# Performance work log

Hardware: AMD Instinct MI355X
Metric: run time of the kernel (lower is better)

The kernel has to match this reference:

```python
import jax, jax.numpy as jnp
import numpy as np

EPS = 1.1920928955078125e-07  # torch fp32 default eps for F.rms_norm
N_HEADS = 16
HEAD_DIM = 128


def apply_rotary_emb(x, cos, sin):
    # x: [B,S,H,D]; cos/sin: [1,S,1,D/2]
    d = x.shape[-1] // 2
    x1, x2 = x[..., :d], x[..., d:]
    return jnp.concatenate([x1 * cos + x2 * sin, -x1 * sin + x2 * cos], axis=-1)


def rms_norm(x):
    # F.rms_norm over last dim, no learned weight
    ms = jnp.mean(jnp.square(x), axis=-1, keepdims=True)
    return x * jax.lax.rsqrt(ms + EPS)


def setup_inputs() -> dict:
    key = jax.random.key(0)
    ks = jax.random.split(key, 7)
    B, S, D = 2, 2048, 2048
    half = HEAD_DIM // 2
    # rotary tables (built like standard RoPE for realism)
    inv_freq = 1.0 / (10000.0 ** (np.arange(0, half, dtype=np.float32) / half))
    t = np.arange(S, dtype=np.float32)
    freqs = np.outer(t, inv_freq)  # [S, D/2]
    cos = jnp.asarray(np.cos(freqs))[None, :, None, :]
    sin = jnp.asarray(np.sin(freqs))[None, :, None, :]
    sd = 1.0 / np.sqrt(D)
    return {
        "x": jax.random.normal(ks[0], (B, S, D), jnp.float32),
        "cos": cos,
        "sin": sin,
        "Wq": jax.random.normal(ks[1], (D, D), jnp.float32) * sd,
        "Wk": jax.random.normal(ks[2], (D, D), jnp.float32) * sd,
        "Wv": jax.random.normal(ks[3], (D, D), jnp.float32) * sd,
        "Wo": jax.random.normal(ks[4], (D, D), jnp.float32) * sd,
    }


def reference(x, cos, sin, Wq, Wk, Wv, Wo):
    B, S, D = x.shape
    H, Hd = N_HEADS, HEAD_DIM
    q = (x @ Wq.T).reshape(B, S, H, Hd)
    k = (x @ Wk.T).reshape(B, S, H, Hd)
    v = (x @ Wv.T).reshape(B, S, H, Hd)
    q = apply_rotary_emb(q, cos[:, :S], sin[:, :S])
    k = apply_rotary_emb(k, cos[:, :S], sin[:, :S])
    q = rms_norm(q) * 1.2  # [B,S,H,Hd]
    k = rms_norm(k) * 1.2
    scale = 1.0 / jnp.sqrt(jnp.asarray(Hd, x.dtype))
    # scores: [B,H,Sq,Sk]
    scores = jnp.einsum("bqhd,bkhd->bhqk", q, k) * scale
    attn = jax.nn.softmax(scores, axis=-1)
    y = jnp.einsum("bhqk,bkhd->bqhd", attn, v).reshape(B, S, D)
    return y @ Wo.T
```

## Files before the change

### kernel.cpp

```cpp
#include <hip/hip_runtime.h>
#include <hip/hip_bf16.h>
#include <math.h>

typedef __bf16 bf16;
typedef __attribute__((ext_vector_type(8))) __bf16 bf16x8;
typedef __attribute__((ext_vector_type(4))) float f32x4;
typedef __attribute__((ext_vector_type(16))) float f32x16;

#define DEV __device__ __forceinline__

DEV void gload16(const void* g, void* l) {
    __builtin_amdgcn_global_load_lds(
        (__attribute__((address_space(1))) void*)(void*)g,
        (__attribute__((address_space(3))) void*)l, 16, 0, 0);
}

DEV unsigned pk2(float a, float b) {
    union { bf16 h[2]; unsigned u; } z;
    z.h[0] = (bf16)a; z.h[1] = (bf16)b;
    return z.u;
}

DEV void plswap(unsigned& a, unsigned& b) {
    asm volatile("v_permlane32_swap_b32 %0, %1" : "+v"(a), "+v"(b));
}

DEV f32x16 mfma32(bf16x8 a, bf16x8 b, f32x16 c) {
    return __builtin_amdgcn_mfma_f32_32x32x16_bf16(a, b, c, 0, 0, 0);
}

__global__ __launch_bounds__(256) void cvt_kernel(const float* __restrict__ in,
                                                  bf16* __restrict__ out, int n8) {
    for (int i = blockIdx.x * 256 + threadIdx.x; i < n8; i += gridDim.x * 256) {
        const float4* p = (const float4*)(in + (size_t)i * 8);
        float4 a = p[0], b = p[1];
        bf16x8 o;
        o[0] = (bf16)a.x; o[1] = (bf16)a.y; o[2] = (bf16)a.z; o[3] = (bf16)a.w;
        o[4] = (bf16)b.x; o[5] = (bf16)b.y; o[6] = (bf16)b.z; o[7] = (bf16)b.w;
        *(bf16x8*)(out + (size_t)i * 8) = o;
    }
}

__global__ __launch_bounds__(256) void cvtw_kernel(const float* __restrict__ w0,
                                                   const float* __restrict__ w1,
                                                   const float* __restrict__ w2,
                                                   const float* __restrict__ w3,
                                                   bf16* __restrict__ out) {
    const float* in = (blockIdx.y == 0) ? w0 : (blockIdx.y == 1) ? w1
                      : (blockIdx.y == 2) ? w2 : w3;
    bf16* o = out + (size_t)blockIdx.y * 4194304;
    for (int i = blockIdx.x * 256 + threadIdx.x; i < 524288; i += 512 * 256) {
        const float4* p = (const float4*)(in + (size_t)i * 8);
        float4 a = p[0], b = p[1];
        bf16x8 v;
        v[0] = (bf16)a.x; v[1] = (bf16)a.y; v[2] = (bf16)a.z; v[3] = (bf16)a.w;
        v[4] = (bf16)b.x; v[5] = (bf16)b.y; v[6] = (bf16)b.z; v[7] = (bf16)b.w;
        *(bf16x8*)(o + (size_t)i * 8) = v;
    }
}

__global__ __launch_bounds__(512, 2) void gemm_qkv(const bf16* __restrict__ A,
                                                   const bf16* __restrict__ Bg,
                                                   bf16* __restrict__ outq) {
    __shared__ __align__(16) bf16 As[3][256 * 32];
    __shared__ __align__(16) bf16 Bs[3][384 * 32];
    const int tid = threadIdx.x, lane = tid & 63, wv = tid >> 6;
    const int q31 = lane & 31, h5 = lane >> 5;
    const int wm = wv >> 2, wn = wv & 3;
    const int K = 2048;

    int lin = blockIdx.x;
    int swz = (lin & 7) * 32 + (lin >> 3);
    const int tm = (swz >> 4) * 256;
    const int tn = (swz & 15) * 384;

    f32x16 acc[4][3] = {};

    auto stageA = [&](int t, int buf) {
#pragma unroll
        for (int l = 0; l < 2; ++l) {
            int chunk = l * 8 + wv;
            int row = chunk * 16 + (lane >> 2);
            int cb = ((lane & 3) * 16) ^ (((row >> 1) & 3) << 4);
            gload16((const char*)(A + (size_t)(tm + row) * K + t * 32) + cb,
                    (char*)(As[buf]) + chunk * 1024);
        }
    };
    auto stageB = [&](int t, int buf) {
#pragma unroll
        for (int l = 0; l < 3; ++l) {
            int chunk = l * 8 + wv;
            int row = chunk * 16 + (lane >> 2);
            int cb = ((lane & 3) * 16) ^ (((row >> 1) & 3) << 4);
            gload16((const char*)(Bg + (size_t)(tn + row) * K + t * 32) + cb,
                    (char*)(Bs[buf]) + chunk * 1024);
        }
    };
    auto rdA = [&](int buf, int mb, int ks) -> bf16x8 {
        int row = wm * 128 + mb * 32 + q31;
        int off = (ks * 32 + h5 * 16) ^ (((row >> 1) & 3) << 4);
        return *(const bf16x8*)((const char*)(As[buf]) + row * 64 + off);
    };
    auto rdB = [&](int buf, int nb, int ks) -> bf16x8 {
        int row = wn * 96 + nb * 32 + q31;
        int off = (ks * 32 + h5 * 16) ^ (((row >> 1) & 3) << 4);
        return *(const bf16x8*)((const char*)(Bs[buf]) + row * 64 + off);
    };

    stageA(0, 0); stageB(0, 0);
    stageA(1, 1); stageB(1, 1);
    asm volatile("s_waitcnt vmcnt(5)" ::: "memory");
    __builtin_amdgcn_s_barrier();

    int cur = 0, nxt2 = 2;
    for (int t = 0; t < 64; ++t) {
        bf16x8 af[2][2], bfr[3][2];
#pragma unroll
        for (int mb = 0; mb < 2; ++mb)
#pragma unroll
            for (int ks = 0; ks < 2; ++ks) af[mb][ks] = rdA(cur, mb, ks);
#pragma unroll
        for (int nb = 0; nb < 3; ++nb)
#pragma unroll
            for (int ks = 0; ks < 2; ++ks) bfr[nb][ks] = rdB(cur, nb, ks);
        if (t < 62) stageA(t + 2, nxt2);
        __builtin_amdgcn_s_barrier();
        asm volatile("s_waitcnt lgkmcnt(0)" ::: "memory");
        __builtin_amdgcn_sched_barrier(0);
        __builtin_amdgcn_s_setprio(1);
#pragma unroll
        for (int mb = 0; mb < 2; ++mb)
#pragma unroll
            for (int nb = 0; nb < 3; ++nb)
#pragma unroll
                for (int ks = 0; ks < 2; ++ks)
                    acc[mb][nb] = mfma32(af[mb][ks], bfr[nb][ks], acc[mb][nb]);
        __builtin_amdgcn_s_setprio(0);
        __builtin_amdgcn_s_barrier();
#pragma unroll
        for (int mb = 0; mb < 2; ++mb)
#pragma unroll
            for (int ks = 0; ks < 2; ++ks) af[mb][ks] = rdA(cur, 2 + mb, ks);
        if (t < 62) stageB(t + 2, nxt2);
        __builtin_amdgcn_s_barrier();
        asm volatile("s_waitcnt lgkmcnt(0)" ::: "memory");
        __builtin_amdgcn_sched_barrier(0);
        __builtin_amdgcn_s_setprio(1);
#pragma unroll
        for (int mb = 0; mb < 2; ++mb)
#pragma unroll
            for (int nb = 0; nb < 3; ++nb)
#pragma unroll
                for (int ks = 0; ks < 2; ++ks)
                    acc[2 + mb][nb] = mfma32(af[mb][ks], bfr[nb][ks], acc[2 + mb][nb]);
        __builtin_amdgcn_s_setprio(0);
        if (t < 62)
            asm volatile("s_waitcnt vmcnt(5)" ::: "memory");
        else
            asm volatile("s_waitcnt vmcnt(0)" ::: "memory");
        __builtin_amdgcn_s_barrier();
        cur = (cur == 2) ? 0 : cur + 1;
        nxt2 = (nxt2 == 2) ? 0 : nxt2 + 1;
    }

#pragma unroll
    for (int mb = 0; mb < 4; ++mb)
#pragma unroll
        for (int nb = 0; nb < 3; ++nb) {
            int colbase = tn + wn * 96 + nb * 32;
            bf16* op = outq + (size_t)(colbase >> 11) * 8388608 +
                       (colbase & 2047) + q31;
#pragma unroll
            for (int r = 0; r < 16; ++r) {
                int row = tm + wm * 128 + mb * 32 + (r & 3) + 8 * (r >> 2) + 4 * h5;
                op[(size_t)row * 2048] = (bf16)acc[mb][nb][r];
            }
        }
}

template <bool F32OUT>
__global__ __launch_bounds__(256) void gemm_bt(const bf16* __restrict__ A,
                                               const bf16* __restrict__ B,
                                               void* __restrict__ Cout,
                                               int M, int N, int K) {
    __shared__ __align__(16) bf16 As[128 * 64];
    __shared__ __align__(16) bf16 Bs[128 * 64];
    const int tid = threadIdx.x, lane = tid & 63, wv = tid >> 6;
    int lin = blockIdx.y * 16 + blockIdx.x;
    int swz = (lin & 7) * 64 + (lin >> 3);
    const int tm = (swz >> 4) * 128, tn = (swz & 15) * 128;
    const int wr = (wv >> 1) * 64, wc = (wv & 1) * 64;

    f32x4 acc[4][4] = {};
    const int scb = (lane & 7) * 16;

    for (int k0 = 0; k0 < K; k0 += 64) {
#pragma unroll
        for (int i = 0; i < 4; ++i) {
            int chunk = wv * 4 + i;
            int row = chunk * 8 + (lane >> 3);
            int cb = scb ^ ((row & 7) << 4);
            gload16((const char*)(A + (size_t)(tm + row) * K + k0) + cb,
                    (char*)As + chunk * 1024);
            gload16((const char*)(B + (size_t)(tn + row) * K + k0) + cb,
                    (char*)Bs + chunk * 1024);
        }
        __syncthreads();
#pragma unroll
        for (int kk = 0; kk < 2; ++kk) {
            bf16x8 af[4], bfr[4];
#pragma unroll
            for (int m = 0; m < 4; ++m) {
                int row = wr + m * 16 + (lane & 15);
                int cb = (kk * 64 + ((lane >> 4) * 16)) ^ ((row & 7) << 4);
                af[m] = *(const bf16x8*)((const char*)As + row * 128 + cb);
            }
#pragma unroll
            for (int n = 0; n < 4; ++n) {
                int row = wc + n * 16 + (lane & 15);
                int cb = (kk * 64 + ((lane >> 4) * 16)) ^ ((row & 7) << 4);
                bfr[n] = *(const bf16x8*)((const char*)Bs + row * 128 + cb);
            }
#pragma unroll
            for (int m = 0; m < 4; ++m)
#pragma unroll
                for (int n = 0; n < 4; ++n)
                    acc[m][n] = __builtin_amdgcn_mfma_f32_16x16x32_bf16(
                        af[m], bfr[n], acc[m][n], 0, 0, 0);
        }
        __syncthreads();
    }
#pragma unroll
    for (int m = 0; m < 4; ++m)
#pragma unroll
        for (int n = 0; n < 4; ++n)
#pragma unroll
            for (int r = 0; r < 4; ++r) {
                int row = tm + wr + m * 16 + (lane >> 4) * 4 + r;
                int col = tn + wc + n * 16 + (lane & 15);
                if (F32OUT)
                    ((float*)Cout)[(size_t)row * N + col] = acc[m][n][r];
                else
                    ((bf16*)Cout)[(size_t)row * N + col] = (bf16)acc[m][n][r];
            }
}

__global__ __launch_bounds__(256) void rope_rms(bf16* __restrict__ q,
                                                bf16* __restrict__ k,
                                                const float* __restrict__ cosp,
                                                const float* __restrict__ sinp) {
    int gw = blockIdx.x * 4 + (threadIdx.x >> 6);
    int lane = threadIdx.x & 63;
    bf16* base = (blockIdx.y == 0) ? q : k;
    int m = gw >> 4, h = gw & 15;
    int s = m & 2047;
    bf16* p = base + (size_t)m * 2048 + h * 128;
    float x1 = (float)p[lane], x2 = (float)p[lane + 64];
    float c = cosp[s * 64 + lane], si = sinp[s * 64 + lane];
    float r1 = x1 * c + x2 * si;
    float r2 = x2 * c - x1 * si;
    float ss = r1 * r1 + r2 * r2;
#pragma unroll
    for (int msk = 1; msk < 64; msk <<= 1) ss += __shfl_xor(ss, msk);
    float sc = rsqrtf(ss * (1.0f / 128.0f) + 1.1920928955078125e-07f) * 1.2f;
    if (blockIdx.y == 0) sc *= (0.08838834764831845f * 1.4426950408889634f);
    p[lane] = (bf16)(r1 * sc);
    p[lane + 64] = (bf16)(r2 * sc);
}

__global__ __launch_bounds__(512, 2) void attn_kernel(const bf16* __restrict__ q,
                                                      const bf16* __restrict__ k,
                                                      const bf16* __restrict__ v,
                                                      bf16* __restrict__ y) {
    __shared__ __align__(16) bf16 Ks[2][64 * 128];
    __shared__ __align__(16) bf16 Vt[2][128][72];

    const int tid = threadIdx.x, lane = tid & 63, wv = tid >> 6;
    const int q31 = lane & 31, h5 = lane >> 5;

    int wgid = blockIdx.y * 8 + blockIdx.x;
    int xcd = wgid & 7, j = wgid >> 3;
    const int bh = xcd * 4 + (j >> 3);
    const int qblk = j & 7;
    const int b = bh >> 4, h = bh & 15;
    const int q0 = qblk * 256;

    const bf16* qptr = q + (size_t)(b * 2048 + q0 + wv * 32 + q31) * 2048 +
                       h * 128 + h5 * 8;
    bf16x8 qf[8];
#pragma unroll
    for (int ks = 0; ks < 8; ++ks) qf[ks] = *(const bf16x8*)(qptr + ks * 16);

    float mrun = -INFINITY, lrun = 0.f;
    f32x16 acco[4] = {};

    const int p = tid & 63, rg = tid >> 6;
    const bf16* vbase = v + (size_t)(b * 2048 + rg * 8) * 2048 + h * 128 + 2 * p;
    const bf16* kbase = k + (size_t)(b * 2048) * 2048 + h * 128;
    const int vx = ((p >> 2) & 1) << 5;

    unsigned u[8];

    auto stageK = [&](int t, int buf) {
#pragma unroll
        for (int i = 0; i < 2; ++i) {
            int chunk = wv * 2 + i;
            int row = chunk * 4 + (lane >> 4);
            int cb = ((lane & 15) * 16) ^ ((row & 7) << 4);
            gload16((const char*)(kbase + (size_t)(t * 64 + row) * 2048) + cb,
                    (char*)(Ks[buf]) + chunk * 1024);
        }
    };
    auto loadV = [&](int t) {
        const bf16* vp = vbase + (size_t)(t * 64) * 2048;
#pragma unroll
        for (int jj = 0; jj < 8; ++jj)
            u[jj] = *(const unsigned*)(vp + (size_t)jj * 2048);
    };
    auto writeV = [&](int buf) {
        union { unsigned short s[8]; bf16x8 v8; } lo, hi;
#pragma unroll
        for (int jj = 0; jj < 8; ++jj) {
            lo.s[jj] = (unsigned short)(u[jj] & 0xffff);
            hi.s[jj] = (unsigned short)(u[jj] >> 16);
        }
        char* r0 = (char*)(&Vt[buf][2 * p][0]);
        char* r1 = (char*)(&Vt[buf][2 * p + 1][0]);
        *(bf16x8*)(r0 + ((rg * 16) ^ vx)) = lo.v8;
        *(bf16x8*)(r1 + ((rg * 16) ^ vx)) = hi.v8;
    };

    stageK(0, 0);
    loadV(0);
    writeV(0);
    __syncthreads();

    const int rx = ((q31 >> 3) & 1) << 5;

    for (int t = 0; t < 32; ++t) {
        const int c = t & 1;
        if (t < 31) {
            stageK(t + 1, c ^ 1);
            loadV(t + 1);
        }

        f32x16 st[2];
        __builtin_amdgcn_s_setprio(1);
#pragma unroll
        for (int kvb = 0; kvb < 2; ++kvb) {
            f32x16 a = {};
#pragma unroll
            for (int ks = 0; ks < 8; ++ks) {
                int row = kvb * 32 + q31;
                int cb = (32 * ks + 16 * h5) ^ ((row & 7) << 4);
                const bf16x8 kf =
                    *(const bf16x8*)((const char*)(Ks[c]) + row * 256 + cb);
                a = __builtin_amdgcn_mfma_f32_32x32x16_bf16(kf, qf[ks], a, 0, 0, 0);
            }
            st[kvb] = a;
        }
        __builtin_amdgcn_s_setprio(0);

        float t8[8];
#pragma unroll
        for (int r = 0; r < 8; ++r)
            t8[r] = fmaxf(fmaxf(st[0][r], st[0][r + 8]),
                          fmaxf(st[1][r], st[1][r + 8]));
        float mx = fmaxf(fmaxf(fmaxf(t8[0], t8[1]), fmaxf(t8[2], t8[3])),
                         fmaxf(fmaxf(t8[4], t8[5]), fmaxf(t8[6], t8[7])));
        mx = fmaxf(mx, __shfl_xor(mx, 32));

        if (__any(mx - mrun > 8.0f)) {
            float mn = fmaxf(mrun, mx);
            float alpha = exp2f(mrun - mn);
            mrun = mn;
            lrun *= alpha;
#pragma unroll
            for (int r = 0; r < 16; ++r) {
                int qr = (r & 3) + 8 * (r >> 2) + 4 * h5;
                float al = __shfl(alpha, qr);
                acco[0][r] *= al; acco[1][r] *= al;
                acco[2][r] *= al; acco[3][r] *= al;
            }
        }

        unsigned w[2][8];
        float rsa = 0.f, rsb = 0.f;
#pragma unroll
        for (int kvb = 0; kvb < 2; ++kvb)
#pragma unroll
            for (int i = 0; i < 8; ++i) {
                float p0 = exp2f(st[kvb][2 * i] - mrun);
                float p1 = exp2f(st[kvb][2 * i + 1] - mrun);
                if (i & 1) rsb += p0 + p1; else rsa += p0 + p1;
                w[kvb][i] = pk2(p0, p1);
            }
        float rs = rsa + rsb;
        rs += __shfl_xor(rs, 32);
        lrun += rs;

        __builtin_amdgcn_s_setprio(1);
#pragma unroll
        for (int b2 = 0; b2 < 2; ++b2)
#pragma unroll
            for (int ksl = 0; ksl < 2; ++ksl) {
                const int ks = b2 * 2 + ksl, u0 = ksl * 4;
                unsigned f0 = w[b2][u0 + 0], f2 = w[b2][u0 + 2];
                unsigned f1 = w[b2][u0 + 1], f3 = w[b2][u0 + 3];
                plswap(f0, f2);
                plswap(f1, f3);
                union { unsigned uu[4]; bf16x8 v8; } fr;
                fr.uu[0] = f0; fr.uu[1] = f1; fr.uu[2] = f2; fr.uu[3] = f3;
#pragma unroll
                for (int dblk = 0; dblk < 4; ++dblk) {
                    const char* vrow = (const char*)(&Vt[c][dblk * 32 + q31][0]);
                    const bf16x8 vf =
                        *(const bf16x8*)(vrow + ((ks * 32 + h5 * 16) ^ rx));
                    acco[dblk] = __builtin_amdgcn_mfma_f32_32x32x16_bf16(
                        fr.v8, vf, acco[dblk], 0, 0, 0);
                }
            }
        __builtin_amdgcn_s_setprio(0);

        if (t < 31) writeV(c ^ 1);
        __syncthreads();
    }

    float linv = 1.0f / lrun;
#pragma unroll
    for (int r = 0; r < 16; ++r) {
        int qr = (r & 3) + 8 * (r >> 2) + 4 * h5;
        float il = __shfl(linv, qr);
        size_t row = (size_t)(b * 2048 + q0 + wv * 32 + qr) * 2048 + h * 128;
#pragma unroll
        for (int dblk = 0; dblk < 4; ++dblk)
            y[row + dblk * 32 + q31] = (bf16)(acco[dblk][r] * il);
    }
}

extern "C" void kernel_launch(void* const* d_in, const int* in_sizes, int n_in,
                              void* d_out, int out_size, void* d_ws, size_t ws_size,
                              hipStream_t stream) {
    const float* x = (const float*)d_in[0];
    const float* cs = (const float*)d_in[1];
    const float* sn = (const float*)d_in[2];
    const float* Wq = (const float*)d_in[3];
    const float* Wk = (const float*)d_in[4];
    const float* Wv = (const float*)d_in[5];
    const float* Wo = (const float*)d_in[6];

    char* ws = (char*)d_ws;
    bf16* xb  = (bf16*)(ws + 0);
    bf16* wqb = (bf16*)(ws + 16777216);
    bf16* wob = (bf16*)(ws + 41943040);
    bf16* qb  = (bf16*)(ws + 50331648);
    bf16* kb  = (bf16*)(ws + 67108864);
    bf16* vb  = (bf16*)(ws + 83886080);
    bf16* yb  = (bf16*)(ws + 100663296);

    cvt_kernel<<<1024, 256, 0, stream>>>(x, xb, 8388608 / 8);
    cvtw_kernel<<<dim3(512, 4), 256, 0, stream>>>(Wq, Wk, Wv, Wo, wqb);

    gemm_qkv<<<256, 512, 0, stream>>>(xb, wqb, qb);

    rope_rms<<<dim3(16384, 2), 256, 0, stream>>>(qb, kb, cs, sn);

    attn_kernel<<<dim3(8, 32), 512, 0, stream>>>(qb, kb, vb, yb);

    dim3 g(16, 32);
    gemm_bt<true><<<g, 256, 0, stream>>>(yb, wob, d_out, 4096, 2048, 2048);
}
```

Baseline: 287.1 us.

## Shrink attention tiles to 128-query blocks with 32-key steps and 4 waves

Restructures the attention kernel so each workgroup has 4 waves covering 128 queries, and the key/value loop advances 32 keys per iteration instead of 64. The grid doubles to 512 workgroups and LDS per block halves, so more blocks fit per CU. The aim is better occupancy and load balance across CUs. In exchange there are twice as many loop iterations and barriers, less MFMA work per iteration to hide load latency, and more K/V re-reads from global memory. The V transpose layout and staging indices are adjusted to the smaller tile.

```diff
diff --git a/kernel.cpp b/kernel.cpp
--- a/kernel.cpp
+++ b/kernel.cpp
@@ -268,22 +268,22 @@
     p[lane + 64] = (bf16)(r2 * sc);
 }
 
-__global__ __launch_bounds__(512, 2) void attn_kernel(const bf16* __restrict__ q,
+__global__ __launch_bounds__(256, 4) void attn_kernel(const bf16* __restrict__ q,
                                                       const bf16* __restrict__ k,
                                                       const bf16* __restrict__ v,
                                                       bf16* __restrict__ y) {
-    __shared__ __align__(16) bf16 Ks[2][64 * 128];
-    __shared__ __align__(16) bf16 Vt[2][128][72];
+    __shared__ __align__(16) bf16 Ks[2][32 * 128];
+    __shared__ __align__(16) bf16 Vt[2][128][40];
 
     const int tid = threadIdx.x, lane = tid & 63, wv = tid >> 6;
     const int q31 = lane & 31, h5 = lane >> 5;
 
-    int wgid = blockIdx.y * 8 + blockIdx.x;
+    int wgid = blockIdx.y * 16 + blockIdx.x;
     int xcd = wgid & 7, j = wgid >> 3;
-    const int bh = xcd * 4 + (j >> 3);
-    const int qblk = j & 7;
+    const int bh = xcd * 4 + (j >> 4);
+    const int qblk = j & 15;
     const int b = bh >> 4, h = bh & 15;
-    const int q0 = qblk * 256;
+    const int q0 = qblk * 128;
 
     const bf16* qptr = q + (size_t)(b * 2048 + q0 + wv * 32 + q31) * 2048 +
                        h * 128 + h5 * 8;
@@ -307,12 +307,12 @@
             int chunk = wv * 2 + i;
             int row = chunk * 4 + (lane >> 4);
             int cb = ((lane & 15) * 16) ^ ((row & 7) << 4);
-            gload16((const char*)(kbase + (size_t)(t * 64 + row) * 2048) + cb,
+            gload16((const char*)(kbase + (size_t)(t * 32 + row) * 2048) + cb,
                     (char*)(Ks[buf]) + chunk * 1024);
         }
     };
     auto loadV = [&](int t) {
-        const bf16* vp = vbase + (size_t)(t * 64) * 2048;
+        const bf16* vp = vbase + (size_t)(t * 32) * 2048;
 #pragma unroll
         for (int jj = 0; jj < 8; ++jj)
             u[jj] = *(const unsigned*)(vp + (size_t)jj * 2048);
@@ -337,35 +337,28 @@
 
     const int rx = ((q31 >> 3) & 1) << 5;
 
-    for (int t = 0; t < 32; ++t) {
+    for (int t = 0; t < 64; ++t) {
         const int c = t & 1;
-        if (t < 31) {
+        if (t < 63) {
             stageK(t + 1, c ^ 1);
             loadV(t + 1);
         }
 
-        f32x16 st[2];
+        f32x16 st = {};
         __builtin_amdgcn_s_setprio(1);
 #pragma unroll
-        for (int kvb = 0; kvb < 2; ++kvb) {
-            f32x16 a = {};
-#pragma unroll
-            for (int ks = 0; ks < 8; ++ks) {
-                int row = kvb * 32 + q31;
-                int cb = (32 * ks + 16 * h5) ^ ((row & 7) << 4);
-                const bf16x8 kf =
-                    *(const bf16x8*)((const char*)(Ks[c]) + row * 256 + cb);
-                a = __builtin_amdgcn_mfma_f32_32x32x16_bf16(kf, qf[ks], a, 0, 0, 0);
-            }
-            st[kvb] = a;
+        for (int ks = 0; ks < 8; ++ks) {
+            int row = q31;
+            int cb = (32 * ks + 16 * h5) ^ ((row & 7) << 4);
+            const bf16x8 kf =
+                *(const bf16x8*)((const char*)(Ks[c]) + row * 256 + cb);
+            st = __builtin_amdgcn_mfma_f32_32x32x16_bf16(kf, qf[ks], st, 0, 0, 0);
         }
         __builtin_amdgcn_s_setprio(0);
 
         float t8[8];
 #pragma unroll
-        for (int r = 0; r < 8; ++r)
-            t8[r] = fmaxf(fmaxf(st[0][r], st[0][r + 8]),
-                          fmaxf(st[1][r], st[1][r + 8]));
+        for (int r = 0; r < 8; ++r) t8[r] = fmaxf(st[r], st[r + 8]);
         float mx = fmaxf(fmaxf(fmaxf(t8[0], t8[1]), fmaxf(t8[2], t8[3])),
                          fmaxf(fmaxf(t8[4], t8[5]), fmaxf(t8[6], t8[7])));
         mx = fmaxf(mx, __shfl_xor(mx, 32));
@@ -384,45 +377,41 @@
             }
         }
 
-        unsigned w[2][8];
+        unsigned w[8];
         float rsa = 0.f, rsb = 0.f;
 #pragma unroll
-        for (int kvb = 0; kvb < 2; ++kvb)
-#pragma unroll
-            for (int i = 0; i < 8; ++i) {
-                float p0 = exp2f(st[kvb][2 * i] - mrun);
-                float p1 = exp2f(st[kvb][2 * i + 1] - mrun);
-                if (i & 1) rsb += p0 + p1; else rsa += p0 + p1;
-                w[kvb][i] = pk2(p0, p1);
-            }
+        for (int i = 0; i < 8; ++i) {
+            float p0 = exp2f(st[2 * i] - mrun);
+            float p1 = exp2f(st[2 * i + 1] - mrun);
+            if (i & 1) rsb += p0 + p1; else rsa += p0 + p1;
+            w[i] = pk2(p0, p1);
+        }
         float rs = rsa + rsb;
         rs += __shfl_xor(rs, 32);
         lrun += rs;
 
         __builtin_amdgcn_s_setprio(1);
 #pragma unroll
-        for (int b2 = 0; b2 < 2; ++b2)
-#pragma unroll
-            for (int ksl = 0; ksl < 2; ++ksl) {
-                const int ks = b2 * 2 + ksl, u0 = ksl * 4;
-                unsigned f0 = w[b2][u0 + 0], f2 = w[b2][u0 + 2];
-                unsigned f1 = w[b2][u0 + 1], f3 = w[b2][u0 + 3];
-                plswap(f0, f2);
-                plswap(f1, f3);
-                union { unsigned uu[4]; bf16x8 v8; } fr;
-                fr.uu[0] = f0; fr.uu[1] = f1; fr.uu[2] = f2; fr.uu[3] = f3;
-#pragma unroll
-                for (int dblk = 0; dblk < 4; ++dblk) {
-                    const char* vrow = (const char*)(&Vt[c][dblk * 32 + q31][0]);
-                    const bf16x8 vf =
-                        *(const bf16x8*)(vrow + ((ks * 32 + h5 * 16) ^ rx));
-                    acco[dblk] = __builtin_amdgcn_mfma_f32_32x32x16_bf16(
-                        fr.v8, vf, acco[dblk], 0, 0, 0);
-                }
-            }
+        for (int ksl = 0; ksl < 2; ++ksl) {
+            const int u0 = ksl * 4;
+            unsigned f0 = w[u0 + 0], f2 = w[u0 + 2];
+            unsigned f1 = w[u0 + 1], f3 = w[u0 + 3];
+            plswap(f0, f2);
+            plswap(f1, f3);
+            union { unsigned uu[4]; bf16x8 v8; } fr;
+            fr.uu[0] = f0; fr.uu[1] = f1; fr.uu[2] = f2; fr.uu[3] = f3;
+#pragma unroll
+            for (int dblk = 0; dblk < 4; ++dblk) {
+                const char* vrow = (const char*)(&Vt[c][dblk * 32 + q31][0]);
+                const bf16x8 vf =
+                    *(const bf16x8*)(vrow + ((ksl * 32 + h5 * 16) ^ rx));
+                acco[dblk] = __builtin_amdgcn_mfma_f32_32x32x16_bf16(
+                    fr.v8, vf, acco[dblk], 0, 0, 0);
+            }
+        }
         __builtin_amdgcn_s_setprio(0);
 
-        if (t < 31) writeV(c ^ 1);
+        if (t < 63) writeV(c ^ 1);
         __syncthreads();
     }
 
@@ -465,7 +454,7 @@
 
     rope_rms<<<dim3(16384, 2), 256, 0, stream>>>(qb, kb, cs, sn);
 
-    attn_kernel<<<dim3(8, 32), 512, 0, stream>>>(qb, kb, vb, yb);
+    attn_kernel<<<dim3(16, 32), 256, 0, stream>>>(qb, kb, vb, yb);
 
     dim3 g(16, 32);
     gemm_bt<true><<<g, 256, 0, stream>>>(yb, wob, d_out, 4096, 2048, 2048);
```

Measured after the change: 389.4 us. 35.6% more time.

## Replace output projection GEMM with triple-buffered 32x32 MFMA pipelined kernel

Applied to the files above, without the earlier changes.

The output projection GEMM is replaced by a dedicated kernel modeled on the QKV GEMM. It uses 256x128 tiles, 512 threads, a three-stage LDS ring with split A/B prefetch interleaved between MFMA phases, and 32x32x16 MFMAs with raised wave priority. The goal is to hide global load latency behind compute and cut barrier stalls, since the old kernel loaded and synchronized every K step with no overlap. The cost is more complex scheduling, a grid of only 256 blocks, and hardcoded sizes.

```diff
diff --git a/kernel.cpp b/kernel.cpp
--- a/kernel.cpp
+++ b/kernel.cpp
@@ -178,71 +178,110 @@
         }
 }
 
-template <bool F32OUT>
-__global__ __launch_bounds__(256) void gemm_bt(const bf16* __restrict__ A,
-                                               const bf16* __restrict__ B,
-                                               void* __restrict__ Cout,
-                                               int M, int N, int K) {
-    __shared__ __align__(16) bf16 As[128 * 64];
-    __shared__ __align__(16) bf16 Bs[128 * 64];
+__global__ __launch_bounds__(512, 2) void gemm_wo(const bf16* __restrict__ A,
+                                                  const bf16* __restrict__ Bg,
+                                                  float* __restrict__ out) {
+    __shared__ __align__(16) bf16 As[3][256 * 32];
+    __shared__ __align__(16) bf16 Bs[3][128 * 32];
     const int tid = threadIdx.x, lane = tid & 63, wv = tid >> 6;
-    int lin = blockIdx.y * 16 + blockIdx.x;
-    int swz = (lin & 7) * 64 + (lin >> 3);
-    const int tm = (swz >> 4) * 128, tn = (swz & 15) * 128;
-    const int wr = (wv >> 1) * 64, wc = (wv & 1) * 64;
-
-    f32x4 acc[4][4] = {};
-    const int scb = (lane & 7) * 16;
-
-    for (int k0 = 0; k0 < K; k0 += 64) {
-#pragma unroll
-        for (int i = 0; i < 4; ++i) {
-            int chunk = wv * 4 + i;
-            int row = chunk * 8 + (lane >> 3);
-            int cb = scb ^ ((row & 7) << 4);
-            gload16((const char*)(A + (size_t)(tm + row) * K + k0) + cb,
-                    (char*)As + chunk * 1024);
-            gload16((const char*)(B + (size_t)(tn + row) * K + k0) + cb,
-                    (char*)Bs + chunk * 1024);
-        }
-        __syncthreads();
-#pragma unroll
-        for (int kk = 0; kk < 2; ++kk) {
-            bf16x8 af[4], bfr[4];
-#pragma unroll
-            for (int m = 0; m < 4; ++m) {
-                int row = wr + m * 16 + (lane & 15);
-                int cb = (kk * 64 + ((lane >> 4) * 16)) ^ ((row & 7) << 4);
-                af[m] = *(const bf16x8*)((const char*)As + row * 128 + cb);
+    const int q31 = lane & 31, h5 = lane >> 5;
+    const int wm = wv >> 1, wn = wv & 1;
+    const int K = 2048;
+
+    int lin = blockIdx.x;
+    int swz = (lin & 7) * 32 + (lin >> 3);
+    const int tm = (swz >> 4) * 256;
+    const int tn = (swz & 15) * 128;
+
+    f32x16 acc[2][2] = {};
+
+    auto stageA = [&](int t, int buf) {
+#pragma unroll
+        for (int l = 0; l < 2; ++l) {
+            int chunk = l * 8 + wv;
+            int row = chunk * 16 + (lane >> 2);
+            int cb = ((lane & 3) * 16) ^ (((row >> 1) & 3) << 4);
+            gload16((const char*)(A + (size_t)(tm + row) * K + t * 32) + cb,
+                    (char*)(As[buf]) + chunk * 1024);
+        }
+    };
+    auto stageB = [&](int t, int buf) {
+        int chunk = wv;
+        int row = chunk * 16 + (lane >> 2);
+        int cb = ((lane & 3) * 16) ^ (((row >> 1) & 3) << 4);
+        gload16((const char*)(Bg + (size_t)(tn + row) * K + t * 32) + cb,
+                (char*)(Bs[buf]) + chunk * 1024);
+    };
+    auto rdA = [&](int buf, int mb, int ks) -> bf16x8 {
+        int row = wm * 64 + mb * 32 + q31;
+        int off = (ks * 32 + h5 * 16) ^ (((row >> 1) & 3) << 4);
+        return *(const bf16x8*)((const char*)(As[buf]) + row * 64 + off);
+    };
+    auto rdB = [&](int buf, int nb, int ks) -> bf16x8 {
+        int row = wn * 64 + nb * 32 + q31;
+        int off = (ks * 32 + h5 * 16) ^ (((row >> 1) & 3) << 4);
+        return *(const bf16x8*)((const char*)(Bs[buf]) + row * 64 + off);
+    };
+
+    stageA(0, 0); stageB(0, 0);
+    stageA(1, 1); stageB(1, 1);
+    asm volatile("s_waitcnt vmcnt(3)" ::: "memory");
+    __builtin_amdgcn_s_barrier();
+
+    int cur = 0, nxt2 = 2;
+    for (int t = 0; t < 64; ++t) {
+        bf16x8 af[2], bfr[2][2];
+#pragma unroll
+        for (int ks = 0; ks < 2; ++ks) af[ks] = rdA(cur, 0, ks);
+#pragma unroll
+        for (int nb = 0; nb < 2; ++nb)
+#pragma unroll
+            for (int ks = 0; ks < 2; ++ks) bfr[nb][ks] = rdB(cur, nb, ks);
+        if (t < 62) stageA(t + 2, nxt2);
+        __builtin_amdgcn_s_barrier();
+        asm volatile("s_waitcnt lgkmcnt(0)" ::: "memory");
+        __builtin_amdgcn_sched_barrier(0);
+        __builtin_amdgcn_s_setprio(1);
+#pragma unroll
+        for (int nb = 0; nb < 2; ++nb)
+#pragma unroll
+            for (int ks = 0; ks < 2; ++ks)
+                acc[0][nb] = mfma32(af[ks], bfr[nb][ks], acc[0][nb]);
+        __builtin_amdgcn_s_setprio(0);
+        __builtin_amdgcn_s_barrier();
+#pragma unroll
+        for (int ks = 0; ks < 2; ++ks) af[ks] = rdA(cur, 1, ks);
+        if (t < 62) stageB(t + 2, nxt2);
+        __builtin_amdgcn_s_barrier();
+        asm volatile("s_waitcnt lgkmcnt(0)" ::: "memory");
+        __builtin_amdgcn_sched_barrier(0);
+        __builtin_amdgcn_s_setprio(1);
+#pragma unroll
+        for (int nb = 0; nb < 2; ++nb)
+#pragma unroll
+            for (int ks = 0; ks < 2; ++ks)
+                acc[1][nb] = mfma32(af[ks], bfr[nb][ks], acc[1][nb]);
+        __builtin_amdgcn_s_setprio(0);
+        if (t < 62)
+            asm volatile("s_waitcnt vmcnt(3)" ::: "memory");
+        else
+            asm volatile("s_waitcnt vmcnt(0)" ::: "memory");
+        __builtin_amdgcn_s_barrier();
+        cur = (cur == 2) ? 0 : cur + 1;
+        nxt2 = (nxt2 == 2) ? 0 : nxt2 + 1;
+    }
+
+#pragma unroll
+    for (int mb = 0; mb < 2; ++mb)
+#pragma unroll
+        for (int nb = 0; nb < 2; ++nb) {
+            int col = tn + wn * 64 + nb * 32 + q31;
+#pragma unroll
+            for (int r = 0; r < 16; ++r) {
+                int row = tm + wm * 64 + mb * 32 + (r & 3) + 8 * (r >> 2) + 4 * h5;
+                out[(size_t)row * 2048 + col] = acc[mb][nb][r];
             }
-#pragma unroll
-            for (int n = 0; n < 4; ++n) {
-                int row = wc + n * 16 + (lane & 15);
-                int cb = (kk * 64 + ((lane >> 4) * 16)) ^ ((row & 7) << 4);
-                bfr[n] = *(const bf16x8*)((const char*)Bs + row * 128 + cb);
-            }
-#pragma unroll
-            for (int m = 0; m < 4; ++m)
-#pragma unroll
-                for (int n = 0; n < 4; ++n)
-                    acc[m][n] = __builtin_amdgcn_mfma_f32_16x16x32_bf16(
-                        af[m], bfr[n], acc[m][n], 0, 0, 0);
-        }
-        __syncthreads();
-    }
-#pragma unroll
-    for (int m = 0; m < 4; ++m)
-#pragma unroll
-        for (int n = 0; n < 4; ++n)
-#pragma unroll
-            for (int r = 0; r < 4; ++r) {
-                int row = tm + wr + m * 16 + (lane >> 4) * 4 + r;
-                int col = tn + wc + n * 16 + (lane & 15);
-                if (F32OUT)
-                    ((float*)Cout)[(size_t)row * N + col] = acc[m][n][r];
-                else
-                    ((bf16*)Cout)[(size_t)row * N + col] = (bf16)acc[m][n][r];
-            }
+        }
 }
 
 __global__ __launch_bounds__(256) void rope_rms(bf16* __restrict__ q,
@@ -467,6 +506,5 @@
 
     attn_kernel<<<dim3(8, 32), 512, 0, stream>>>(qb, kb, vb, yb);
 
-    dim3 g(16, 32);
-    gemm_bt<true><<<g, 256, 0, stream>>>(yb, wob, d_out, 4096, 2048, 2048);
-}
+    gemm_wo<<<256, 512, 0, stream>>>(yb, wob, (float*)d_out);
+}
```

After: 296.5 us. 1.03x slower.
